# Optimization experiments

Measured on AMD Instinct MI355X. Metric: run time of the kernel, lower is better.

## Reference

```python
import jax, jax.numpy as jnp
import numpy as np

D_MODEL = 1024
N_HEADS = 16
HEAD = D_MODEL // N_HEADS  # 64


def setup_inputs() -> dict:
    key = jax.random.key(0)
    ks = jax.random.split(key, 6)
    B, T = 2, 2048
    x = jax.random.normal(ks[0], (B, T, D_MODEL), dtype=jnp.float32)
    s_in = 1.0 / np.sqrt(HEAD)
    # per-head projections: Linear(head_size -> d_model), no bias. Stored as [H, head, d_model].
    Wq = jax.random.normal(ks[1], (N_HEADS, HEAD, D_MODEL), dtype=jnp.float32) * s_in
    Wk = jax.random.normal(ks[2], (N_HEADS, HEAD, D_MODEL), dtype=jnp.float32) * s_in
    Wv = jax.random.normal(ks[3], (N_HEADS, HEAD, D_MODEL), dtype=jnp.float32) * s_in
    # output projection: Linear(H*d_model -> d_model) with bias
    Wo = jax.random.normal(ks[4], (N_HEADS * D_MODEL, D_MODEL), dtype=jnp.float32) / np.sqrt(N_HEADS * D_MODEL)
    bo = jax.random.normal(ks[5], (D_MODEL,), dtype=jnp.float32) * 0.01
    return {"x": x, "Wq": Wq, "Wk": Wk, "Wv": Wv, "Wo": Wo, "bo": bo}


def reference(x, Wq, Wk, Wv, Wo, bo):
    B, T, _ = x.shape
    # split into per-head slices: [B, H, T, head]
    xh = x.reshape(B, T, N_HEADS, HEAD).transpose(0, 2, 1, 3)
    q = jnp.einsum("bhtd,hdm->bhtm", xh, Wq)  # [B,H,T,d_model]
    k = jnp.einsum("bhtd,hdm->bhtm", xh, Wk)
    v = jnp.einsum("bhtd,hdm->bhtm", xh, Wv)
    # scale uses D = head input dim (= HEAD), per the original code
    scores = jnp.einsum("bhtm,bhsm->bhts", q, k) / jnp.sqrt(jnp.asarray(HEAD, x.dtype))
    weights = jax.nn.softmax(scores, axis=-1)
    vb = jnp.einsum("bhts,bhsm->bhtm", weights, v)  # [B,H,T,d_model]
    cat = vb.transpose(0, 2, 1, 3).reshape(B, T, N_HEADS * D_MODEL)
    return cat @ Wo + bo
```

## Files before the change

### kernel.cpp

```cpp
#include <hip/hip_runtime.h>
#include <math.h>

typedef unsigned u32;
typedef unsigned short u16;
typedef __attribute__((ext_vector_type(8))) __bf16 bf16x8;
typedef __attribute__((ext_vector_type(4))) float f32x4;

#define DEVI __device__ __forceinline__

DEVI u16 f2bf(float f) {
    u32 u = __builtin_bit_cast(u32, f);
    u += 0x7fffu + ((u >> 16) & 1u);
    return (u16)(u >> 16);
}

DEVI u32 packbf(float a, float b) {
    u32 ua = __builtin_bit_cast(u32, a) + 0x8000u;
    u32 ub = __builtin_bit_cast(u32, b) + 0x8000u;
    return (ua >> 16) | (ub & 0xffff0000u);
}

DEVI bf16x8 ldsf(const u16* p) { return *(const bf16x8*)p; }

DEVI f32x4 mfma16(bf16x8 a, bf16x8 b, f32x4 c) {
    return __builtin_amdgcn_mfma_f32_16x16x32_bf16(a, b, c, 0, 0, 0);
}

#if __has_builtin(__builtin_amdgcn_exp2f)
DEVI float fexp2(float x) { return __builtin_amdgcn_exp2f(x); }
#else
DEVI float fexp2(float x) { return exp2f(x); }
#endif

__global__ __launch_bounds__(256) void k_pw(const float* __restrict__ x,
                                            const float* __restrict__ Wq, const float* __restrict__ Wk,
                                            const float* __restrict__ Wv, const float* __restrict__ Wo,
                                            u16* __restrict__ xswz, u16* __restrict__ xt2,
                                            u16* __restrict__ mtg, u16* __restrict__ W2) {
    __shared__ __align__(16) char SM[18432];
    const int tid = threadIdx.x;
    const int id = blockIdx.x;
    const int rr = tid >> 2, c16 = (tid & 3) * 16;

    if (id < 272) {
        u16* LA = (u16*)SM;
        u16* LB = (u16*)(SM + 9216);
        const int w = tid >> 6, lane = tid & 63, g = lane >> 4, ln = lane & 15;
        f32x4 acc[4] = {};
        float4 pa[4], pb[4];

        if (id >= 256) {
            const int h = id - 256;
            {
                const float4* sa = (const float4*)(Wk + (h * 64 + rr) * 1024 + c16);
                const float4* sb = (const float4*)(Wq + (h * 64 + rr) * 1024 + c16);
#pragma unroll
                for (int j = 0; j < 4; j++) { pa[j] = sa[j]; pb[j] = sb[j]; }
            }
            for (int kb = 0; kb < 16; kb++) {
                __syncthreads();
                {
                    union { uint4 q[2]; u16 s[16]; } ua, ub;
#pragma unroll
                    for (int j = 0; j < 4; j++) {
                        ua.s[j*4+0]=f2bf(pa[j].x); ua.s[j*4+1]=f2bf(pa[j].y); ua.s[j*4+2]=f2bf(pa[j].z); ua.s[j*4+3]=f2bf(pa[j].w);
                        ub.s[j*4+0]=f2bf(pb[j].x); ub.s[j*4+1]=f2bf(pb[j].y); ub.s[j*4+2]=f2bf(pb[j].z); ub.s[j*4+3]=f2bf(pb[j].w);
                    }
                    *(uint4*)(LA + rr * 72 + c16) = ua.q[0]; *(uint4*)(LA + rr * 72 + c16 + 8) = ua.q[1];
                    *(uint4*)(LB + rr * 72 + c16) = ub.q[0]; *(uint4*)(LB + rr * 72 + c16 + 8) = ub.q[1];
                }
                __syncthreads();
                if (kb < 15) {
                    const float4* sa = (const float4*)(Wk + (h * 64 + rr) * 1024 + (kb + 1) * 64 + c16);
                    const float4* sb = (const float4*)(Wq + (h * 64 + rr) * 1024 + (kb + 1) * 64 + c16);
#pragma unroll
                    for (int j = 0; j < 4; j++) { pa[j] = sa[j]; pb[j] = sb[j]; }
                }
#pragma unroll
                for (int ks = 0; ks < 2; ks++) {
                    bf16x8 bb = ldsf(LB + (w * 16 + ln) * 72 + ks * 32 + g * 8);
#pragma unroll
                    for (int mt = 0; mt < 4; mt++) {
                        bf16x8 a = ldsf(LA + (mt * 16 + ln) * 72 + ks * 32 + g * 8);
                        acc[mt] = mfma16(a, bb, acc[mt]);
                    }
                }
            }
#pragma unroll
            for (int mt = 0; mt < 4; mt++)
#pragma unroll
                for (int r = 0; r < 4; r++)
                    mtg[h * 4096 + (mt * 16 + g * 4 + r) * 64 + w * 16 + ln] =
                        f2bf(acc[mt][r] * 0.18033688011112f);
        } else {
            const int h = id >> 4, n0 = (id & 15) * 64;
            {
                const float4* sa = (const float4*)(Wo + (h * 1024 + rr) * 1024 + n0 + c16);
                const float4* sb = (const float4*)(Wv + (h * 64 + rr) * 1024 + c16);
#pragma unroll
                for (int j = 0; j < 4; j++) { pa[j] = sa[j]; pb[j] = sb[j]; }
            }
            for (int kb = 0; kb < 16; kb++) {
                __syncthreads();
                {
                    union { uint4 q[2]; u16 s[16]; } ub;
#pragma unroll
                    for (int j = 0; j < 4; j++) {
                        ub.s[j*4+0]=f2bf(pb[j].x); ub.s[j*4+1]=f2bf(pb[j].y); ub.s[j*4+2]=f2bf(pb[j].z); ub.s[j*4+3]=f2bf(pb[j].w);
                    }
                    *(uint4*)(LB + rr * 72 + c16) = ub.q[0]; *(uint4*)(LB + rr * 72 + c16 + 8) = ub.q[1];
#pragma unroll
                    for (int j = 0; j < 4; j++) {
                        LA[(c16 + j * 4 + 0) * 72 + rr] = f2bf(pa[j].x);
                        LA[(c16 + j * 4 + 1) * 72 + rr] = f2bf(pa[j].y);
                        LA[(c16 + j * 4 + 2) * 72 + rr] = f2bf(pa[j].z);
                        LA[(c16 + j * 4 + 3) * 72 + rr] = f2bf(pa[j].w);
                    }
                }
                __syncthreads();
                if (kb < 15) {
                    const float4* sa = (const float4*)(Wo + (h * 1024 + (kb + 1) * 64 + rr) * 1024 + n0 + c16);
                    const float4* sb = (const float4*)(Wv + (h * 64 + rr) * 1024 + (kb + 1) * 64 + c16);
#pragma unroll
                    for (int j = 0; j < 4; j++) { pa[j] = sa[j]; pb[j] = sb[j]; }
                }
#pragma unroll
                for (int ks = 0; ks < 2; ks++) {
                    bf16x8 bb = ldsf(LB + (w * 16 + ln) * 72 + ks * 32 + g * 8);
#pragma unroll
                    for (int mt = 0; mt < 4; mt++) {
                        bf16x8 a = ldsf(LA + (mt * 16 + ln) * 72 + ks * 32 + g * 8);
                        acc[mt] = mfma16(a, bb, acc[mt]);
                    }
                }
            }
            int d = w * 16 + ln;
#pragma unroll
            for (int mt = 0; mt < 4; mt++)
#pragma unroll
                for (int r = 0; r < 4; r++) {
                    int n = n0 + mt * 16 + g * 4 + r;
                    W2[h * 65536 + n * 64 + (((d >> 3) ^ (n & 7)) << 3) + (d & 7)] = f2bf(acc[mt][r]);
                }
        }
    } else {
        const int pid = id - 272;
        const int kt = pid & 31, h = (pid >> 5) & 15, b = pid >> 9, bh = b * 16 + h;
        float* T = (float*)SM;
        int t = kt * 64 + rr;
        const float4* gx = (const float4*)(x + (b * 2048 + t) * 1024 + h * 64 + c16);
        float4 f[4];
#pragma unroll
        for (int j = 0; j < 4; j++) f[j] = gx[j];
#pragma unroll
        for (int j = 0; j < 4; j++) {
            T[rr * 65 + c16 + j * 4 + 0] = f[j].x; T[rr * 65 + c16 + j * 4 + 1] = f[j].y;
            T[rr * 65 + c16 + j * 4 + 2] = f[j].z; T[rr * 65 + c16 + j * 4 + 3] = f[j].w;
        }
        {
            union { uint4 q[2]; u16 s[16]; } u;
#pragma unroll
            for (int j = 0; j < 4; j++) {
                u.s[j * 4 + 0] = f2bf(f[j].x); u.s[j * 4 + 1] = f2bf(f[j].y);
                u.s[j * 4 + 2] = f2bf(f[j].z); u.s[j * 4 + 3] = f2bf(f[j].w);
            }
            u16* dst = xswz + (bh * 2048 + t) * 64;
            int c0 = (tid & 3) * 2, sw = rr & 7;
            *(uint4*)(dst + ((c0 ^ sw) << 3))       = u.q[0];
            *(uint4*)(dst + (((c0 + 1) ^ sw) << 3)) = u.q[1];
        }
        __syncthreads();
        int dd = tid >> 2, t4 = (tid & 3) * 16;
        union { uint2 d2[4]; u16 s[16]; } ou;
#pragma unroll
        for (int j = 0; j < 16; j++) ou.s[j] = f2bf(T[(t4 + j) * 65 + dd]);
        u16* dst = xt2 + bh * 131072 + kt * 4096 + dd * 64;
        const int nt0 = t4 >> 4;
        const int cb = (nt0 >> 1) * 4;
        const int off = (nt0 & 1) * 4;
        const int sw = dd & 7;
#pragma unroll
        for (int g4 = 0; g4 < 4; g4++) {
            int c = cb + g4;
            *(uint2*)(dst + ((c ^ sw) << 3) + off) = ou.d2[g4];
        }
    }
}

__global__ __launch_bounds__(256, 2) void k_attn(const u16* __restrict__ xswz, const u16* __restrict__ xt2,
                                                 const u16* __restrict__ mtg, u16* __restrict__ U2) {
    __shared__ __align__(16) u16 smem[16384];
    u16* KB = smem;
    u16* VB = smem + 8192;

    const int tid = threadIdx.x;
    const int w = tid >> 6, lane = tid & 63, g = lane >> 4, ln = lane & 15, ln7 = lane & 7;
    const int qt = blockIdx.x, h = blockIdx.y, b = blockIdx.z, bh = b * 16 + h;
    const u16* xs = xswz + bh * 131072;
    const u16* xv = xt2 + bh * 131072;

    bf16x8 qf[2][2];
    {
        u16* LM  = smem;
        u16* LXQ = smem + 4608;
        {
            int r4 = tid >> 2, c4 = (tid & 3) * 2;
            const uint4* gm = (const uint4*)(mtg + h * 4096 + r4 * 64);
            uint4 m0 = gm[c4], m1 = gm[c4 + 1];
            *(uint4*)(LM + r4 * 72 + c4 * 8)     = m0;
            *(uint4*)(LM + r4 * 72 + c4 * 8 + 8) = m1;
            int r2 = tid >> 1, c2 = (tid & 1) * 4;
            const uint4* gx = (const uint4*)(xs + (qt * 128 + r2) * 64);
            uint4 x0 = gx[c2], x1 = gx[c2 + 1], x2 = gx[c2 + 2], x3 = gx[c2 + 3];
            *(uint4*)(LXQ + r2 * 72 + c2 * 8)      = x0;
            *(uint4*)(LXQ + r2 * 72 + c2 * 8 + 8)  = x1;
            *(uint4*)(LXQ + r2 * 72 + c2 * 8 + 16) = x2;
            *(uint4*)(LXQ + r2 * 72 + c2 * 8 + 24) = x3;
        }
        __syncthreads();
        f32x4 acc[2][4] = {};
#pragma unroll
        for (int qh = 0; qh < 2; qh++) {
            int row = qh * 64 + w * 16 + ln;
#pragma unroll
            for (int ks = 0; ks < 2; ks++) {
                bf16x8 a = ldsf(LXQ + row * 72 + (((ks * 4 + g) ^ ln7) << 3));
#pragma unroll
                for (int nt = 0; nt < 4; nt++) {
                    bf16x8 bb = ldsf(LM + (nt * 16 + ln) * 72 + ks * 32 + g * 8);
                    acc[qh][nt] = mfma16(a, bb, acc[qh][nt]);
                }
            }
        }
        __syncthreads();
#pragma unroll
        for (int qh = 0; qh < 2; qh++) {
            u16* QLw = smem + qh * 4608 + w * 1152;
#pragma unroll
            for (int nt = 0; nt < 4; nt++)
#pragma unroll
                for (int r = 0; r < 4; r++)
                    QLw[(g * 4 + r) * 72 + nt * 16 + ln] = f2bf(acc[qh][nt][r]);
        }
        asm volatile("s_waitcnt lgkmcnt(0)" ::: "memory");
#pragma unroll
        for (int qh = 0; qh < 2; qh++) {
            u16* QLw = smem + qh * 4608 + w * 1152;
            qf[qh][0] = ldsf(QLw + ln * 72 + g * 8);
            qf[qh][1] = ldsf(QLw + ln * 72 + 32 + g * 8);
        }
        __syncthreads();
    }

    {
        const uint4* gk = (const uint4*)xs;
        const uint4* gv = (const uint4*)xv;
        uint4 k0 = gk[tid], k1 = gk[tid + 256], v0 = gv[tid], v1 = gv[tid + 256];
        uint4* lk = (uint4*)KB;
        uint4* lv = (uint4*)VB;
        lk[tid] = k0; lk[tid + 256] = k1; lv[tid] = v0; lv[tid + 256] = v1;
    }
    __syncthreads();

    float lrow[2] = {0.f, 0.f};
    f32x4 o[2][4] = {};

#pragma unroll 2
    for (int kt = 0; kt < 32; ++kt) {
        const int cur = (kt & 1) << 12;
        const u16* KL = KB + cur;
        const u16* VL = VB + cur;

        uint4 kr0, kr1, vr0, vr1;
        if (kt + 1 < 32) {
            const uint4* gk = (const uint4*)(xs + (kt + 1) * 4096);
            const uint4* gv = (const uint4*)(xv + (kt + 1) * 4096);
            kr0 = gk[tid]; kr1 = gk[tid + 256]; vr0 = gv[tid]; vr1 = gv[tid + 256];
        }

        f32x4 s[2][4] = {};
        __builtin_amdgcn_s_setprio(1);
#pragma unroll
        for (int ks = 0; ks < 2; ks++) {
#pragma unroll
            for (int nt = 0; nt < 4; nt++) {
                bf16x8 a = ldsf(KL + (nt * 16 + ln) * 64 + (((ks * 4 + g) ^ ln7) << 3));
                s[0][nt] = mfma16(a, qf[0][ks], s[0][nt]);
                s[1][nt] = mfma16(a, qf[1][ks], s[1][nt]);
            }
        }
        __builtin_amdgcn_s_setprio(0);

        u32 pk[2][4][2];
#pragma unroll
        for (int qh = 0; qh < 2; qh++) {
            float ts = 0.f;
#pragma unroll
            for (int nt = 0; nt < 4; nt++) {
                float p0 = fexp2(s[qh][nt][0]), p1 = fexp2(s[qh][nt][1]);
                float p2 = fexp2(s[qh][nt][2]), p3 = fexp2(s[qh][nt][3]);
                pk[qh][nt][0] = packbf(p0, p1);
                pk[qh][nt][1] = packbf(p2, p3);
                ts += (p0 + p1) + (p2 + p3);
            }
            lrow[qh] += ts;
        }

        __builtin_amdgcn_s_setprio(1);
#pragma unroll
        for (int ks = 0; ks < 2; ks++) {
            union { u32 u[4]; bf16x8 v; } pf[2];
#pragma unroll
            for (int qh = 0; qh < 2; qh++) {
                pf[qh].u[0] = pk[qh][2 * ks][0];
                pf[qh].u[1] = pk[qh][2 * ks][1];
                pf[qh].u[2] = pk[qh][2 * ks + 1][0];
                pf[qh].u[3] = pk[qh][2 * ks + 1][1];
            }
#pragma unroll
            for (int dt = 0; dt < 4; dt++) {
                bf16x8 a = ldsf(VL + (dt * 16 + ln) * 64 + (((ks * 4 + g) ^ ln7) << 3));
                o[0][dt] = mfma16(a, pf[0].v, o[0][dt]);
                o[1][dt] = mfma16(a, pf[1].v, o[1][dt]);
            }
        }
        __builtin_amdgcn_s_setprio(0);

        if (kt + 1 < 32) {
            const int nxt = cur ^ 4096;
            uint4* lk = (uint4*)(KB + nxt);
            uint4* lv = (uint4*)(VB + nxt);
            lk[tid] = kr0; lk[tid + 256] = kr1; lv[tid] = vr0; lv[tid + 256] = vr1;
        }
        __syncthreads();
    }

#pragma unroll
    for (int qh = 0; qh < 2; qh++) {
        lrow[qh] += __shfl_xor(lrow[qh], 16, 64);
        lrow[qh] += __shfl_xor(lrow[qh], 32, 64);
        float inv = 1.0f / lrow[qh];
        int t = b * 2048 + qt * 128 + qh * 64 + w * 16 + ln;
#pragma unroll
        for (int dt = 0; dt < 4; dt++) {
            ushort4 vv;
            vv.x = f2bf(o[qh][dt][0] * inv); vv.y = f2bf(o[qh][dt][1] * inv);
            vv.z = f2bf(o[qh][dt][2] * inv); vv.w = f2bf(o[qh][dt][3] * inv);
            int c = dt * 2 + (g >> 1);
            int pos = c ^ (t & 7);
            *(ushort4*)(U2 + h * 262144 + t * 64 + pos * 8 + (g & 1) * 4) = vv;
        }
    }
}

__global__ __launch_bounds__(256) void k_out(const u16* __restrict__ U2, const u16* __restrict__ W2,
                                             const float* __restrict__ bo, float* __restrict__ out) {
    __shared__ __align__(16) u16 AL[8192], BL[8192];
    const int tid = threadIdx.x;
    const int w = tid >> 6, lane = tid & 63, g = lane >> 4, ln = lane & 15;
    const int n0 = blockIdx.x * 128, r0 = blockIdx.y * 128;
    const int rw = (w >> 1) * 64, cw = (w & 1) * 64;
    f32x4 acc[4][4] = {};
    uint4 ar[4], br[4];
    {
        const uint4* ga = (const uint4*)(U2 + r0 * 64);
        const uint4* gb = (const uint4*)(W2 + n0 * 64);
#pragma unroll
        for (int i = 0; i < 4; i++) { ar[i] = ga[tid + 256 * i]; br[i] = gb[tid + 256 * i]; }
    }
    for (int kb = 0; kb < 16; kb++) {
        __syncthreads();
        {
            uint4* la = (uint4*)AL;
            uint4* lb = (uint4*)BL;
#pragma unroll
            for (int i = 0; i < 4; i++) { la[tid + 256 * i] = ar[i]; lb[tid + 256 * i] = br[i]; }
        }
        __syncthreads();
        if (kb + 1 < 16) {
            const uint4* ga = (const uint4*)(U2 + (kb + 1) * 262144 + r0 * 64);
            const uint4* gb = (const uint4*)(W2 + (kb + 1) * 65536 + n0 * 64);
#pragma unroll
            for (int i = 0; i < 4; i++) { ar[i] = ga[tid + 256 * i]; br[i] = gb[tid + 256 * i]; }
        }
#pragma unroll
        for (int ks = 0; ks < 2; ks++) {
            bf16x8 af[4], bfr[4];
#pragma unroll
            for (int mt = 0; mt < 4; mt++) {
                int rr = rw + mt * 16 + ln;
                af[mt] = ldsf(AL + rr * 64 + (((ks * 4 + g) ^ (rr & 7)) << 3));
            }
#pragma unroll
            for (int nt = 0; nt < 4; nt++) {
                int rr = cw + nt * 16 + ln;
                bfr[nt] = ldsf(BL + rr * 64 + (((ks * 4 + g) ^ (rr & 7)) << 3));
            }
#pragma unroll
            for (int mt = 0; mt < 4; mt++)
#pragma unroll
                for (int nt = 0; nt < 4; nt++)
                    acc[mt][nt] = mfma16(af[mt], bfr[nt], acc[mt][nt]);
        }
    }
#pragma unroll
    for (int nt = 0; nt < 4; nt++) {
        int col = n0 + cw + nt * 16 + ln;
        float bias = bo[col];
#pragma unroll
        for (int mt = 0; mt < 4; mt++)
#pragma unroll
            for (int r = 0; r < 4; r++)
                out[(r0 + rw + mt * 16 + g * 4 + r) * 1024 + col] = acc[mt][nt][r] + bias;
    }
}

extern "C" void kernel_launch(void* const* d_in, const int* in_sizes, int n_in,
                              void* d_out, int out_size, void* d_ws, size_t ws_size,
                              hipStream_t stream) {
    const float* x  = (const float*)d_in[0];
    const float* Wq = (const float*)d_in[1];
    const float* Wk = (const float*)d_in[2];
    const float* Wv = (const float*)d_in[3];
    const float* Wo = (const float*)d_in[4];
    const float* bo = (const float*)d_in[5];
    float* out = (float*)d_out;

    char* ws = (char*)d_ws;
    u16* xswz = (u16*)(ws);
    u16* mtg  = (u16*)(ws + 8388608);
    u16* xt2  = (u16*)(ws + 8519680);
    u16* W2   = (u16*)(ws + 16908288);
    u16* U2   = (u16*)(ws + 19005440);

    k_pw<<<1296, 256, 0, stream>>>(x, Wq, Wk, Wv, Wo, xswz, xt2, mtg, W2);
    k_attn<<<dim3(16, 16, 2), 256, 0, stream>>>(xswz, xt2, mtg, U2);
    k_out<<<dim3(8, 32), 256, 0, stream>>>(U2, W2, bo, out);
}
```

Before: 237.2 us.

## Shrink output GEMM tiles to 64x64 and stage results through LDS for vector stores

The output projection kernel moves from 128x128 tiles to 64x64 tiles, so the grid grows from 256 to 1024 blocks and the work spreads over more CUs. The epilogue now writes each wave's accumulators to a padded shared-memory scratch area, then reads them back as float4 and writes coalesced float4 rows with the bias added. This replaces scattered scalar stores. In exchange, each loaded byte is reused less, so global and L2 traffic for operand tiles per output rises.

```diff
diff --git a/kernel.cpp b/kernel.cpp
--- a/kernel.cpp
+++ b/kernel.cpp
@@ -355,63 +355,71 @@
 
 __global__ __launch_bounds__(256) void k_out(const u16* __restrict__ U2, const u16* __restrict__ W2,
                                              const float* __restrict__ bo, float* __restrict__ out) {
-    __shared__ __align__(16) u16 AL[8192], BL[8192];
+    __shared__ __align__(16) u16 AL[4096], BL[4096];
+    __shared__ __align__(16) float SC[4608];
     const int tid = threadIdx.x;
     const int w = tid >> 6, lane = tid & 63, g = lane >> 4, ln = lane & 15;
-    const int n0 = blockIdx.x * 128, r0 = blockIdx.y * 128;
-    const int rw = (w >> 1) * 64, cw = (w & 1) * 64;
-    f32x4 acc[4][4] = {};
-    uint4 ar[4], br[4];
+    const int n0 = blockIdx.x * 64, r0 = blockIdx.y * 64;
+    const int rw = (w >> 1) * 32, cw = (w & 1) * 32;
+    f32x4 acc[2][2] = {};
+    uint4 ar[2], br[2];
     {
         const uint4* ga = (const uint4*)(U2 + r0 * 64);
         const uint4* gb = (const uint4*)(W2 + n0 * 64);
-#pragma unroll
-        for (int i = 0; i < 4; i++) { ar[i] = ga[tid + 256 * i]; br[i] = gb[tid + 256 * i]; }
+        ar[0] = ga[tid]; ar[1] = ga[tid + 256];
+        br[0] = gb[tid]; br[1] = gb[tid + 256];
     }
     for (int kb = 0; kb < 16; kb++) {
         __syncthreads();
         {
-            uint4* la = (uint4*)AL;
-            uint4* lb = (uint4*)BL;
-#pragma unroll
-            for (int i = 0; i < 4; i++) { la[tid + 256 * i] = ar[i]; lb[tid + 256 * i] = br[i]; }
+            ((uint4*)AL)[tid] = ar[0]; ((uint4*)AL)[tid + 256] = ar[1];
+            ((uint4*)BL)[tid] = br[0]; ((uint4*)BL)[tid + 256] = br[1];
         }
         __syncthreads();
         if (kb + 1 < 16) {
             const uint4* ga = (const uint4*)(U2 + (kb + 1) * 262144 + r0 * 64);
             const uint4* gb = (const uint4*)(W2 + (kb + 1) * 65536 + n0 * 64);
-#pragma unroll
-            for (int i = 0; i < 4; i++) { ar[i] = ga[tid + 256 * i]; br[i] = gb[tid + 256 * i]; }
+            ar[0] = ga[tid]; ar[1] = ga[tid + 256];
+            br[0] = gb[tid]; br[1] = gb[tid + 256];
         }
 #pragma unroll
         for (int ks = 0; ks < 2; ks++) {
-            bf16x8 af[4], bfr[4];
-#pragma unroll
-            for (int mt = 0; mt < 4; mt++) {
+            bf16x8 af[2], bfr[2];
+#pragma unroll
+            for (int mt = 0; mt < 2; mt++) {
                 int rr = rw + mt * 16 + ln;
                 af[mt] = ldsf(AL + rr * 64 + (((ks * 4 + g) ^ (rr & 7)) << 3));
             }
 #pragma unroll
-            for (int nt = 0; nt < 4; nt++) {
+            for (int nt = 0; nt < 2; nt++) {
                 int rr = cw + nt * 16 + ln;
                 bfr[nt] = ldsf(BL + rr * 64 + (((ks * 4 + g) ^ (rr & 7)) << 3));
             }
 #pragma unroll
-            for (int mt = 0; mt < 4; mt++)
-#pragma unroll
-                for (int nt = 0; nt < 4; nt++)
+            for (int mt = 0; mt < 2; mt++)
+#pragma unroll
+                for (int nt = 0; nt < 2; nt++)
                     acc[mt][nt] = mfma16(af[mt], bfr[nt], acc[mt][nt]);
         }
     }
-#pragma unroll
-    for (int nt = 0; nt < 4; nt++) {
-        int col = n0 + cw + nt * 16 + ln;
-        float bias = bo[col];
-#pragma unroll
-        for (int mt = 0; mt < 4; mt++)
+    float* Wp = SC + w * 1152;
+#pragma unroll
+    for (int mt = 0; mt < 2; mt++)
+#pragma unroll
+        for (int nt = 0; nt < 2; nt++)
 #pragma unroll
             for (int r = 0; r < 4; r++)
-                out[(r0 + rw + mt * 16 + g * 4 + r) * 1024 + col] = acc[mt][nt][r] + bias;
+                Wp[(mt * 16 + g * 4 + r) * 36 + nt * 16 + ln] = acc[mt][nt][r];
+    asm volatile("s_waitcnt lgkmcnt(0)" ::: "memory");
+    const int qd = lane & 7, rbase = lane >> 3;
+    const int col = n0 + cw + qd * 4;
+    const float4 b4 = *(const float4*)(bo + col);
+#pragma unroll
+    for (int i = 0; i < 4; i++) {
+        int row = rbase + 8 * i;
+        float4 v = *(const float4*)(Wp + row * 36 + qd * 4);
+        v.x += b4.x; v.y += b4.y; v.z += b4.z; v.w += b4.w;
+        *(float4*)(out + (r0 + rw + row) * 1024 + col) = v;
     }
 }
 
@@ -435,5 +443,5 @@
 
     k_pw<<<1296, 256, 0, stream>>>(x, Wq, Wk, Wv, Wo, xswz, xt2, mtg, W2);
     k_attn<<<dim3(16, 16, 2), 256, 0, stream>>>(xswz, xt2, mtg, U2);
-    k_out<<<dim3(8, 32), 256, 0, stream>>>(U2, W2, bo, out);
-}
+    k_out<<<dim3(16, 64), 256, 0, stream>>>(U2, W2, bo, out);
+}
```

Result: slower. 259.1 us (+9.2%).
